# Kernel optimization log

Hardware: AMD Instinct MI355X
Metric: run time of the kernel (lower is better)

The kernel has to match this reference:

```python
import jax, jax.numpy as jnp
import numpy as np

NEG = -1e9

def setup_inputs() -> dict:
    key = jax.random.key(0)
    kx, kq, kk, kv, kbq, kbk, kbv = jax.random.split(key, 7)
    B, S, E, D = 4, 2048, 1024, 64
    x = jax.random.normal(kx, (B, S, E), dtype=jnp.float32)
    # causal mask, broadcast over batch (mask == 0 positions get -1e9)
    mask = jnp.broadcast_to(jnp.tril(jnp.ones((S, S), dtype=jnp.int32)), (B, S, S))
    scale = 1.0 / np.sqrt(E)
    Wq = jax.random.normal(kq, (E, D), dtype=jnp.float32) * scale
    Wk = jax.random.normal(kk, (E, D), dtype=jnp.float32) * scale
    Wv = jax.random.normal(kv, (E, D), dtype=jnp.float32) * scale
    bq = jnp.zeros((D,), dtype=jnp.float32)
    bk = jnp.zeros((D,), dtype=jnp.float32)
    bv = jnp.zeros((D,), dtype=jnp.float32)
    return {"x": x, "mask": mask, "Wq": Wq, "bq": bq, "Wk": Wk, "bk": bk, "Wv": Wv, "bv": bv}

def reference(x, mask, Wq, bq, Wk, bk, Wv, bv):
    # Faithful to original: forward passes (K(x), Q(x), V(x)) into sdpa,
    # so the K-projection plays the 'query' role and Q-projection the 'key' role.
    q = jnp.einsum('bse,ed->bsd', x, Wk) + bk  # K(x) used as queries
    k = jnp.einsum('bse,ed->bsd', x, Wq) + bq  # Q(x) used as keys
    v = jnp.einsum('bse,ed->bsd', x, Wv) + bv
    d = q.shape[-1]
    scores = jnp.einsum('bsd,btd->bst', q, k) / jnp.sqrt(jnp.asarray(d, q.dtype))
    scores = jnp.where(mask == 0, jnp.asarray(NEG, scores.dtype), scores)
    weights = jax.nn.softmax(scores, axis=-1)
    return jnp.einsum('bst,btd->bsd', weights, v)
```

## Files before the change

kernel.cpp:

```cpp
#include <hip/hip_runtime.h>

typedef short bf16x8 __attribute__((ext_vector_type(8)));
typedef float f32x4  __attribute__((ext_vector_type(4)));
typedef int   i32x4  __attribute__((ext_vector_type(4)));

#define NEG_BIG (-1e9f)

__device__ __forceinline__ float bf2f(unsigned short h){
  union { unsigned u; float f; } v; v.u = ((unsigned)h) << 16; return v.f;
}
__device__ __forceinline__ unsigned short f2bf(float f){
  union { float f; unsigned u; } v; v.f = f;
  unsigned u = v.u;
  return (unsigned short)((u + 0x7FFFu + ((u >> 16) & 1u)) >> 16);
}

__global__ __launch_bounds__(256) void prep_kernel(
    const float* __restrict__ Wq, const float* __restrict__ bq,
    const float* __restrict__ Wk, const float* __restrict__ bk,
    const float* __restrict__ Wv, const float* __restrict__ bv,
    unsigned short* __restrict__ Wimg, float* __restrict__ bias,
    unsigned int* __restrict__ tick)
{
  int idx = blockIdx.x * 256 + threadIdx.x;
  if (idx < 192 * 1024) {
    int kb2 = idx / 24576, rem = idx % 24576;
    int r = rem >> 7, kk = rem & 127;
    int k = kb2 * 128 + kk;
    float v;
    if (r < 64)       v = Wk[k * 64 + r];
    else if (r < 128) v = Wq[k * 64 + (r - 64)];
    else              v = Wv[k * 64 + (r - 128)];
    Wimg[kb2 * 24576 + r * 128 + kk] = f2bf(v);
  }
  if (idx < 192) {
    float b;
    if (idx < 64)       b = bk[idx];
    else if (idx < 128) b = bq[idx - 64];
    else                b = bv[idx - 128];
    bias[idx] = b;
  }
  if (idx < 128) tick[idx] = 0u;
}

__global__ __launch_bounds__(256, 2) void proj_kernel(
    const float* __restrict__ x,
    const unsigned short* __restrict__ Wimg,
    const float* __restrict__ bias,
    unsigned short* __restrict__ Qh,
    unsigned short* __restrict__ Kh, unsigned short* __restrict__ Vth)
{
  __shared__ __align__(16) unsigned short Axb[32 * 128];
  __shared__ __align__(16) unsigned short Wc[96 * 128];

  const int tid  = threadIdx.x;
  const int lane = tid & 63;
  const int w    = tid >> 6;
  const int rh   = w & 1;
  const int cg   = w >> 1;
  const int quad = lane >> 4;
  const int li   = lane & 15;
  const int rowbase = (blockIdx.x >> 1) * 32;
  const int ch      = blockIdx.x & 1;

  const int xr0 = tid >> 4,          xc0 = tid & 15;
  const int xr1 = (tid + 256) >> 4,  xc1 = tid & 15;
  const float* agp0 = x + (size_t)(rowbase + xr0) * 1024 + xc0 * 8;
  const float* agp1 = x + (size_t)(rowbase + xr1) * 1024 + xc1 * 8;
  const int aslot0 = xr0 * 128 + (xc0 ^ (xr0 & 15)) * 8;
  const int aslot1 = xr1 * 128 + (xc1 ^ (xr1 & 15)) * 8;

  int wslot[6];
  const unsigned short* wgp[6];
  #pragma unroll
  for (int j = 0; j < 6; j++) {
    int cid = tid + j * 256;
    int wr = cid >> 4, c = cid & 15;
    wslot[j] = wr * 128 + (c ^ (wr & 15)) * 8;
    wgp[j] = Wimg + (size_t)(ch * 96 + wr) * 128 + c * 8;
  }

  f32x4 acc[3];
  #pragma unroll
  for (int c = 0; c < 3; c++) acc[c] = (f32x4){0.f, 0.f, 0.f, 0.f};

  const int alr = rh * 16 + li;

  f32x4 rA[4];
  rA[0] = *(const f32x4*)(agp0);
  rA[1] = *(const f32x4*)(agp0 + 4);
  rA[2] = *(const f32x4*)(agp1);
  rA[3] = *(const f32x4*)(agp1 + 4);
  i32x4 rW[6];
  #pragma unroll
  for (int j = 0; j < 6; j++) rW[j] = *(const i32x4*)(wgp[j]);

  for (int ks = 0; ks < 8; ks++) {
    bf16x8 xa, xb;
    #pragma unroll
    for (int j = 0; j < 4; j++) {
      xa[j]     = f2bf(rA[0][j]);
      xa[4 + j] = f2bf(rA[1][j]);
      xb[j]     = f2bf(rA[2][j]);
      xb[4 + j] = f2bf(rA[3][j]);
    }
    __syncthreads();
    *(bf16x8*)&Axb[aslot0] = xa;
    *(bf16x8*)&Axb[aslot1] = xb;
    #pragma unroll
    for (int j = 0; j < 6; j++) *(i32x4*)&Wc[wslot[j]] = rW[j];
    if (ks < 7) {
      rA[0] = *(const f32x4*)(agp0 + (ks + 1) * 128);
      rA[1] = *(const f32x4*)(agp0 + (ks + 1) * 128 + 4);
      rA[2] = *(const f32x4*)(agp1 + (ks + 1) * 128);
      rA[3] = *(const f32x4*)(agp1 + (ks + 1) * 128 + 4);
      #pragma unroll
      for (int j = 0; j < 6; j++)
        rW[j] = *(const i32x4*)(wgp[j] + (size_t)(ks + 1) * 24576);
    }
    __syncthreads();

    #pragma unroll
    for (int sub = 0; sub < 4; sub++) {
      bf16x8 af = *(const bf16x8*)&Axb[alr * 128 + ((sub * 4 + quad) ^ (alr & 15)) * 8];
      #pragma unroll
      for (int ct = 0; ct < 3; ct++) {
        const int lw = cg * 48 + ct * 16 + li;
        bf16x8 bf = *(const bf16x8*)&Wc[lw * 128 + ((sub * 4 + quad) ^ (lw & 15)) * 8];
        acc[ct] = __builtin_amdgcn_mfma_f32_16x16x32_bf16(af, bf, acc[ct], 0, 0, 0);
      }
    }
  }

  #pragma unroll
  for (int ct = 0; ct < 3; ct++)
    #pragma unroll
    for (int r = 0; r < 4; r++) {
      int row = rowbase + rh * 16 + quad * 4 + r;
      int col = ch * 96 + cg * 48 + ct * 16 + li;
      unsigned short h = f2bf(acc[ct][r] + bias[col]);
      if (col < 64)        Qh[(size_t)row * 64 + col] = h;
      else if (col < 128)  Kh[(size_t)row * 64 + (col - 64)] = h;
      else {
        int d = col - 128; int bb = row >> 11; int s = row & 2047;
        Vth[(size_t)bb * 131072 + (size_t)d * 2048 + s] = h;
      }
    }
}

__global__ __launch_bounds__(256, 3) void attn_kernel(
    const unsigned short* __restrict__ Qh,
    const unsigned short* __restrict__ Kh,
    const unsigned short* __restrict__ Vth,
    float* __restrict__ pacc, float* __restrict__ pl,
    unsigned int* __restrict__ tick, float* __restrict__ out)
{
  __shared__ __align__(16) unsigned short Kst[64 * 64];
  __shared__ __align__(16) unsigned short Vst[64 * 64];
  __shared__ __align__(16) unsigned short Ps[4][16 * 72];
  __shared__ unsigned int lastflag;

  const int tid  = threadIdx.x;
  const int lane = tid & 63;
  const int w    = tid >> 6;
  const int quad = lane >> 4;
  const int li   = lane & 15;

  const int b = blockIdx.x / 144;
  int r = blockIdx.x % 144;
  int qg = 31, part = 0;
  #pragma unroll 1
  for (int g = 31; g >= 0; g--) {
    int Pg = (g + 4) >> 2;
    if (r < Pg) { qg = g; part = r; break; }
    r -= Pg;
  }
  const int nkt = qg + 1;
  const int P   = (qg + 4) >> 2;
  const int base = nkt / P, rem = nkt % P;
  const int kt0 = part * base + (part < rem ? part : rem);
  const int kt1 = kt0 + base + (part < rem ? 1 : 0);
  const int qbase = qg * 64 + w * 16;

  size_t qoff = ((size_t)(b * 2048 + qbase) + li) * 64 + quad * 8;
  bf16x8 qh0 = *(const bf16x8*)(Qh + qoff);
  bf16x8 qh1 = *(const bf16x8*)(Qh + qoff + 32);

  f32x4 acc[4];
  #pragma unroll
  for (int c = 0; c < 4; c++) acc[c] = (f32x4){0.f, 0.f, 0.f, 0.f};
  f32x4 lacc = (f32x4){0.f, 0.f, 0.f, 0.f};

  bf16x8 ones;
  #pragma unroll
  for (int j = 0; j < 8; j++) ones[j] = (short)0x3F80;

  const int srow = tid >> 2, sc = tid & 3;
  const unsigned short* kgp = Kh + (size_t)(b * 2048 + srow) * 64 + sc * 8;
  const unsigned short* vgp = Vth + (size_t)b * 131072 + (size_t)srow * 2048 + sc * 8;
  const int ks0 = srow * 64 + ((sc)     ^ (srow & 7)) * 8;
  const int ks1 = srow * 64 + ((sc + 4) ^ (srow & 7)) * 8;

  i32x4 rk0 = *(const i32x4*)(kgp + (size_t)kt0 * 4096);
  i32x4 rk1 = *(const i32x4*)(kgp + (size_t)kt0 * 4096 + 32);
  i32x4 rv0 = *(const i32x4*)(vgp + kt0 * 64);
  i32x4 rv1 = *(const i32x4*)(vgp + kt0 * 64 + 32);

  for (int kt = kt0; kt < kt1; kt++) {
    __syncthreads();
    *(i32x4*)&Kst[ks0] = rk0;
    *(i32x4*)&Kst[ks1] = rk1;
    *(i32x4*)&Vst[ks0] = rv0;
    *(i32x4*)&Vst[ks1] = rv1;
    if (kt + 1 < kt1) {
      rk0 = *(const i32x4*)(kgp + (size_t)(kt + 1) * 4096);
      rk1 = *(const i32x4*)(kgp + (size_t)(kt + 1) * 4096 + 32);
      rv0 = *(const i32x4*)(vgp + (kt + 1) * 64);
      rv1 = *(const i32x4*)(vgp + (kt + 1) * 64 + 32);
    }
    __syncthreads();

    f32x4 s[4];
    #pragma unroll
    for (int c = 0; c < 4; c++) s[c] = (f32x4){0.f, 0.f, 0.f, 0.f};
    __builtin_amdgcn_s_setprio(1);
    #pragma unroll
    for (int ct = 0; ct < 4; ct++) {
      const int n = ct * 16 + li;
      bf16x8 kf0 = *(const bf16x8*)&Kst[n * 64 + ((quad)     ^ (n & 7)) * 8];
      bf16x8 kf1 = *(const bf16x8*)&Kst[n * 64 + ((quad + 4) ^ (n & 7)) * 8];
      s[ct] = __builtin_amdgcn_mfma_f32_16x16x32_bf16(qh0, kf0, s[ct], 0, 0, 0);
      s[ct] = __builtin_amdgcn_mfma_f32_16x16x32_bf16(qh1, kf1, s[ct], 0, 0, 0);
    }
    __builtin_amdgcn_s_setprio(0);

    const bool diag = (kt == qg);
    const int kb = kt * 64;
    #pragma unroll
    for (int ct = 0; ct < 4; ct++)
      #pragma unroll
      for (int rr = 0; rr < 4; rr++) {
        float t = fmaf(s[ct][rr], 0.18033688011112042f, -23.083120654223414f);
        if (diag && (kb + ct * 16 + li > qbase + quad * 4 + rr)) t = -1e30f;
        Ps[w][(quad * 4 + rr) * 72 + ct * 16 + li] = f2bf(exp2f(t));
      }

    bf16x8 ap0 = *(const bf16x8*)&Ps[w][li * 72 + quad * 8];
    bf16x8 ap1 = *(const bf16x8*)&Ps[w][li * 72 + 32 + quad * 8];

    __builtin_amdgcn_s_setprio(1);
    lacc = __builtin_amdgcn_mfma_f32_16x16x32_bf16(ap0, ones, lacc, 0, 0, 0);
    lacc = __builtin_amdgcn_mfma_f32_16x16x32_bf16(ap1, ones, lacc, 0, 0, 0);
    #pragma unroll
    for (int ct = 0; ct < 4; ct++) {
      const int n = ct * 16 + li;
      bf16x8 vf0 = *(const bf16x8*)&Vst[n * 64 + ((quad)     ^ (n & 7)) * 8];
      bf16x8 vf1 = *(const bf16x8*)&Vst[n * 64 + ((quad + 4) ^ (n & 7)) * 8];
      acc[ct] = __builtin_amdgcn_mfma_f32_16x16x32_bf16(ap0, vf0, acc[ct], 0, 0, 0);
      acc[ct] = __builtin_amdgcn_mfma_f32_16x16x32_bf16(ap1, vf1, acc[ct], 0, 0, 0);
    }
    __builtin_amdgcn_s_setprio(0);
  }

  if (P == 1) {
    float inv[4];
    #pragma unroll
    for (int rr = 0; rr < 4; rr++) inv[rr] = 1.0f / lacc[rr];
    #pragma unroll
    for (int ct = 0; ct < 4; ct++)
      #pragma unroll
      for (int rr = 0; rr < 4; rr++)
        out[(size_t)(b * 2048 + qg * 64 + w * 16 + quad * 4 + rr) * 64 + ct * 16 + li]
          = acc[ct][rr] * inv[rr];
    return;
  }

  const int slot = (b * 32 + qg) * 8 + part;
  float* pa = pacc + (size_t)slot * 4096;
  #pragma unroll
  for (int ct = 0; ct < 4; ct++)
    #pragma unroll
    for (int rr = 0; rr < 4; rr++)
      pa[(w * 16 + quad * 4 + rr) * 64 + ct * 16 + li] = acc[ct][rr];
  if (li == 0) {
    #pragma unroll
    for (int rr = 0; rr < 4; rr++)
      pl[slot * 64 + w * 16 + quad * 4 + rr] = lacc[rr];
  }

  __syncthreads();
  if (tid == 0) {
    __threadfence();
    lastflag = (atomicAdd(tick + (b * 32 + qg), 1u) == (unsigned)(P - 1)) ? 1u : 0u;
  }
  __syncthreads();
  if (!lastflag) return;
  __builtin_amdgcn_fence(__ATOMIC_ACQUIRE, "agent");

  const int mr = tid >> 2;
  const int c0 = (tid & 3) * 16;
  const int slot0 = (b * 32 + qg) * 8;
  f32x4 a0 = (f32x4){0.f,0.f,0.f,0.f}, a1 = a0, a2 = a0, a3 = a0;
  float L = 0.f;
  for (int p = 0; p < P; p++) {
    const float* q = pacc + (size_t)(slot0 + p) * 4096 + mr * 64 + c0;
    a0 += *(const f32x4*)(q);
    a1 += *(const f32x4*)(q + 4);
    a2 += *(const f32x4*)(q + 8);
    a3 += *(const f32x4*)(q + 12);
    L += pl[(slot0 + p) * 64 + mr];
  }
  float inv = 1.f / L;
  float* o = out + ((size_t)(b * 2048 + qg * 64 + mr)) * 64 + c0;
  *(f32x4*)(o)      = a0 * inv;
  *(f32x4*)(o + 4)  = a1 * inv;
  *(f32x4*)(o + 8)  = a2 * inv;
  *(f32x4*)(o + 12) = a3 * inv;
}

extern "C" void kernel_launch(void* const* d_in, const int* in_sizes, int n_in,
                              void* d_out, int out_size, void* d_ws, size_t ws_size,
                              hipStream_t stream)
{
  (void)in_sizes; (void)n_in; (void)out_size; (void)ws_size;
  const float* x  = (const float*)d_in[0];
  const float* Wq = (const float*)d_in[2];
  const float* bq = (const float*)d_in[3];
  const float* Wk = (const float*)d_in[4];
  const float* bk = (const float*)d_in[5];
  const float* Wv = (const float*)d_in[6];
  const float* bv = (const float*)d_in[7];
  float* out = (float*)d_out;

  char* ws = (char*)d_ws;
  const size_t MB = 1u << 20;
  unsigned short* Qh   = (unsigned short*)(ws);
  unsigned short* Kh   = (unsigned short*)(ws + 2 * MB);
  unsigned short* Vth  = (unsigned short*)(ws + 4 * MB);
  unsigned short* Wimg = (unsigned short*)(ws + 6 * MB);
  float*          bias = (float*)(ws + 6 * MB + 786432);
  float*          pacc = (float*)(ws + 8 * MB);
  float*          pl   = (float*)(ws + 25 * MB);
  unsigned int*   tick = (unsigned int*)(ws + 26 * MB);

  prep_kernel<<<dim3(768), dim3(256), 0, stream>>>(Wq, bq, Wk, bk, Wv, bv, Wimg, bias, tick);
  proj_kernel<<<dim3(512), dim3(256), 0, stream>>>(x, Wimg, bias, Qh, Kh, Vth);
  attn_kernel<<<dim3(576), dim3(256), 0, stream>>>(Qh, Kh, Vth, pacc, pl, tick, out);
}
```

Measured before the change: 173.1 us.

## Double-buffer attention K/V tiles, split merge into separate kernel, coalesce V^T stores

The attention loop now uses two LDS buffers for K and V, so the next tile is written after compute and only one barrier is needed per iteration instead of two. The atomic last-block merge is replaced by a separate merge kernel launched over query groups with more than one partition. This removes the tick counters and fences at the cost of an extra launch. The projection kernel stages the transposed V tile through shared memory, turning scattered 2-byte transposed stores into 16-byte coalesced ones.

```diff
diff --git a/kernel.cpp b/kernel.cpp
--- a/kernel.cpp
+++ b/kernel.cpp
@@ -19,8 +19,7 @@
     const float* __restrict__ Wq, const float* __restrict__ bq,
     const float* __restrict__ Wk, const float* __restrict__ bk,
     const float* __restrict__ Wv, const float* __restrict__ bv,
-    unsigned short* __restrict__ Wimg, float* __restrict__ bias,
-    unsigned int* __restrict__ tick)
+    unsigned short* __restrict__ Wimg, float* __restrict__ bias)
 {
   int idx = blockIdx.x * 256 + threadIdx.x;
   if (idx < 192 * 1024) {
@@ -40,7 +39,6 @@
     else                b = bv[idx - 128];
     bias[idx] = b;
   }
-  if (idx < 128) tick[idx] = 0u;
 }
 
 __global__ __launch_bounds__(256, 2) void proj_kernel(
@@ -132,33 +130,50 @@
     }
   }
 
-  #pragma unroll
-  for (int ct = 0; ct < 3; ct++)
-    #pragma unroll
-    for (int r = 0; r < 4; r++) {
-      int row = rowbase + rh * 16 + quad * 4 + r;
-      int col = ch * 96 + cg * 48 + ct * 16 + li;
-      unsigned short h = f2bf(acc[ct][r] + bias[col]);
-      if (col < 64)        Qh[(size_t)row * 64 + col] = h;
-      else if (col < 128)  Kh[(size_t)row * 64 + (col - 64)] = h;
-      else {
-        int d = col - 128; int bb = row >> 11; int s = row & 2047;
-        Vth[(size_t)bb * 131072 + (size_t)d * 2048 + s] = h;
+  if (ch == 0) {
+    #pragma unroll
+    for (int ct = 0; ct < 3; ct++)
+      #pragma unroll
+      for (int r = 0; r < 4; r++) {
+        int row = rowbase + rh * 16 + quad * 4 + r;
+        int col = cg * 48 + ct * 16 + li;
+        unsigned short h = f2bf(acc[ct][r] + bias[col]);
+        if (col < 64) Qh[(size_t)row * 64 + col] = h;
+        else          Kh[(size_t)row * 64 + (col - 64)] = h;
       }
-    }
-}
-
-__global__ __launch_bounds__(256, 3) void attn_kernel(
+  } else {
+    __syncthreads();
+    unsigned short* Vlds = Wc;
+    #pragma unroll
+    for (int ct = 0; ct < 3; ct++)
+      #pragma unroll
+      for (int r = 0; r < 4; r++) {
+        int srow = rh * 16 + quad * 4 + r;
+        int col = 96 + cg * 48 + ct * 16 + li;
+        unsigned short h = f2bf(acc[ct][r] + bias[col]);
+        if (col < 128) Kh[(size_t)(rowbase + srow) * 64 + (col - 64)] = h;
+        else           Vlds[(col - 128) * 40 + srow] = h;
+      }
+    __syncthreads();
+    const int d  = tid >> 2;
+    const int sc = tid & 3;
+    bf16x8 vv = *(const bf16x8*)&Vlds[d * 40 + sc * 8];
+    const int grow = rowbase;
+    const int bb = grow >> 11, s0 = (grow & 2047) + sc * 8;
+    *(bf16x8*)&Vth[(size_t)bb * 131072 + (size_t)d * 2048 + s0] = vv;
+  }
+}
+
+__global__ __launch_bounds__(256, 3) void attn_part_kernel(
     const unsigned short* __restrict__ Qh,
     const unsigned short* __restrict__ Kh,
     const unsigned short* __restrict__ Vth,
     float* __restrict__ pacc, float* __restrict__ pl,
-    unsigned int* __restrict__ tick, float* __restrict__ out)
-{
-  __shared__ __align__(16) unsigned short Kst[64 * 64];
-  __shared__ __align__(16) unsigned short Vst[64 * 64];
+    float* __restrict__ out)
+{
+  __shared__ __align__(16) unsigned short Kst[2][64 * 64];
+  __shared__ __align__(16) unsigned short Vst[2][64 * 64];
   __shared__ __align__(16) unsigned short Ps[4][16 * 72];
-  __shared__ unsigned int lastflag;
 
   const int tid  = threadIdx.x;
   const int lane = tid & 63;
@@ -206,19 +221,21 @@
   i32x4 rv0 = *(const i32x4*)(vgp + kt0 * 64);
   i32x4 rv1 = *(const i32x4*)(vgp + kt0 * 64 + 32);
 
+  *(i32x4*)&Kst[0][ks0] = rk0;
+  *(i32x4*)&Kst[0][ks1] = rk1;
+  *(i32x4*)&Vst[0][ks0] = rv0;
+  *(i32x4*)&Vst[0][ks1] = rv1;
+  __syncthreads();
+
+  int cur = 0;
   for (int kt = kt0; kt < kt1; kt++) {
-    __syncthreads();
-    *(i32x4*)&Kst[ks0] = rk0;
-    *(i32x4*)&Kst[ks1] = rk1;
-    *(i32x4*)&Vst[ks0] = rv0;
-    *(i32x4*)&Vst[ks1] = rv1;
-    if (kt + 1 < kt1) {
+    const bool more = (kt + 1 < kt1);
+    if (more) {
       rk0 = *(const i32x4*)(kgp + (size_t)(kt + 1) * 4096);
       rk1 = *(const i32x4*)(kgp + (size_t)(kt + 1) * 4096 + 32);
       rv0 = *(const i32x4*)(vgp + (kt + 1) * 64);
       rv1 = *(const i32x4*)(vgp + (kt + 1) * 64 + 32);
     }
-    __syncthreads();
 
     f32x4 s[4];
     #pragma unroll
@@ -227,8 +244,8 @@
     #pragma unroll
     for (int ct = 0; ct < 4; ct++) {
       const int n = ct * 16 + li;
-      bf16x8 kf0 = *(const bf16x8*)&Kst[n * 64 + ((quad)     ^ (n & 7)) * 8];
-      bf16x8 kf1 = *(const bf16x8*)&Kst[n * 64 + ((quad + 4) ^ (n & 7)) * 8];
+      bf16x8 kf0 = *(const bf16x8*)&Kst[cur][n * 64 + ((quad)     ^ (n & 7)) * 8];
+      bf16x8 kf1 = *(const bf16x8*)&Kst[cur][n * 64 + ((quad + 4) ^ (n & 7)) * 8];
       s[ct] = __builtin_amdgcn_mfma_f32_16x16x32_bf16(qh0, kf0, s[ct], 0, 0, 0);
       s[ct] = __builtin_amdgcn_mfma_f32_16x16x32_bf16(qh1, kf1, s[ct], 0, 0, 0);
     }
@@ -254,12 +271,21 @@
     #pragma unroll
     for (int ct = 0; ct < 4; ct++) {
       const int n = ct * 16 + li;
-      bf16x8 vf0 = *(const bf16x8*)&Vst[n * 64 + ((quad)     ^ (n & 7)) * 8];
-      bf16x8 vf1 = *(const bf16x8*)&Vst[n * 64 + ((quad + 4) ^ (n & 7)) * 8];
+      bf16x8 vf0 = *(const bf16x8*)&Vst[cur][n * 64 + ((quad)     ^ (n & 7)) * 8];
+      bf16x8 vf1 = *(const bf16x8*)&Vst[cur][n * 64 + ((quad + 4) ^ (n & 7)) * 8];
       acc[ct] = __builtin_amdgcn_mfma_f32_16x16x32_bf16(ap0, vf0, acc[ct], 0, 0, 0);
       acc[ct] = __builtin_amdgcn_mfma_f32_16x16x32_bf16(ap1, vf1, acc[ct], 0, 0, 0);
     }
     __builtin_amdgcn_s_setprio(0);
+
+    if (more) {
+      *(i32x4*)&Kst[cur ^ 1][ks0] = rk0;
+      *(i32x4*)&Kst[cur ^ 1][ks1] = rk1;
+      *(i32x4*)&Vst[cur ^ 1][ks0] = rv0;
+      *(i32x4*)&Vst[cur ^ 1][ks1] = rv1;
+      __syncthreads();
+      cur ^= 1;
+    }
   }
 
   if (P == 1) {
@@ -287,31 +313,32 @@
     for (int rr = 0; rr < 4; rr++)
       pl[slot * 64 + w * 16 + quad * 4 + rr] = lacc[rr];
   }
-
-  __syncthreads();
-  if (tid == 0) {
-    __threadfence();
-    lastflag = (atomicAdd(tick + (b * 32 + qg), 1u) == (unsigned)(P - 1)) ? 1u : 0u;
-  }
-  __syncthreads();
-  if (!lastflag) return;
-  __builtin_amdgcn_fence(__ATOMIC_ACQUIRE, "agent");
-
-  const int mr = tid >> 2;
-  const int c0 = (tid & 3) * 16;
+}
+
+__global__ __launch_bounds__(256) void attn_merge_kernel(
+    const float* __restrict__ pacc, const float* __restrict__ pl,
+    float* __restrict__ out)
+{
+  const int tid = threadIdx.x;
+  const int b   = blockIdx.x / 28;
+  const int qg  = (blockIdx.x % 28) + 4;
+  const int rr  = tid >> 2;
+  const int c0  = (tid & 3) * 16;
+  const int P   = (qg + 4) >> 2;
   const int slot0 = (b * 32 + qg) * 8;
+
   f32x4 a0 = (f32x4){0.f,0.f,0.f,0.f}, a1 = a0, a2 = a0, a3 = a0;
   float L = 0.f;
   for (int p = 0; p < P; p++) {
-    const float* q = pacc + (size_t)(slot0 + p) * 4096 + mr * 64 + c0;
-    a0 += *(const f32x4*)(q);
-    a1 += *(const f32x4*)(q + 4);
-    a2 += *(const f32x4*)(q + 8);
-    a3 += *(const f32x4*)(q + 12);
-    L += pl[(slot0 + p) * 64 + mr];
+    const float* pa = pacc + (size_t)(slot0 + p) * 4096 + rr * 64 + c0;
+    a0 += *(const f32x4*)(pa);
+    a1 += *(const f32x4*)(pa + 4);
+    a2 += *(const f32x4*)(pa + 8);
+    a3 += *(const f32x4*)(pa + 12);
+    L += pl[(slot0 + p) * 64 + rr];
   }
   float inv = 1.f / L;
-  float* o = out + ((size_t)(b * 2048 + qg * 64 + mr)) * 64 + c0;
+  float* o = out + ((size_t)(b * 2048 + qg * 64 + rr)) * 64 + c0;
   *(f32x4*)(o)      = a0 * inv;
   *(f32x4*)(o + 4)  = a1 * inv;
   *(f32x4*)(o + 8)  = a2 * inv;
@@ -341,9 +368,9 @@
   float*          bias = (float*)(ws + 6 * MB + 786432);
   float*          pacc = (float*)(ws + 8 * MB);
   float*          pl   = (float*)(ws + 25 * MB);
-  unsigned int*   tick = (unsigned int*)(ws + 26 * MB);
-
-  prep_kernel<<<dim3(768), dim3(256), 0, stream>>>(Wq, bq, Wk, bk, Wv, bv, Wimg, bias, tick);
+
+  prep_kernel<<<dim3(768), dim3(256), 0, stream>>>(Wq, bq, Wk, bk, Wv, bv, Wimg, bias);
   proj_kernel<<<dim3(512), dim3(256), 0, stream>>>(x, Wimg, bias, Qh, Kh, Vth);
-  attn_kernel<<<dim3(576), dim3(256), 0, stream>>>(Qh, Kh, Vth, pacc, pl, tick, out);
-}
+  attn_part_kernel<<<dim3(576), dim3(256), 0, stream>>>(Qh, Kh, Vth, pacc, pl, out);
+  attn_merge_kernel<<<dim3(112), dim3(256), 0, stream>>>(pacc, pl, out);
+}
```

New measurement: 150.6 us. -13.0%, faster.
